# Performance work log

Hardware: AMD Instinct MI355X
Metric: run time of the kernel (lower is better)

Reference implementation:

```python
import jax, jax.numpy as jnp
import numpy as np

B, T1, T2, D = 16, 64, 64, 1024
PROJ = D // 2


def setup_inputs() -> dict:
    key = jax.random.key(0)
    k1, k2, k3 = jax.random.split(key, 3)
    x = jax.random.normal(k1, (B, T1, T2, D), dtype=jnp.float32)
    # glorot-style scale for params
    W_proj = jax.random.normal(k2, (D, PROJ), dtype=jnp.float32) * (2.0 / (D + PROJ)) ** 0.5
    v_score = jax.random.normal(k3, (PROJ,), dtype=jnp.float32) * (1.0 / PROJ) ** 0.5
    return {"x": x, "W_proj": W_proj, "v_score": v_score}


def reference(x, W_proj, v_score):
    # proj_input = tanh(tensordot(x, W_proj, axes=(3,0)))  -> (B, T1, T2, PROJ)
    proj = jnp.tanh(jnp.einsum('btsd,dp->btsp', x, W_proj))
    # att_scores = tensordot(proj, v_score, axes=(3,0))    -> (B, T1, T2)
    scores = jnp.einsum('btsp,p->bts', proj, v_score)
    # softmax over last axis (T2), weighted sum of x over T2 -> (B, T1, D)
    attn = jax.nn.softmax(scores, axis=-1)
    out = jnp.einsum('bts,btsd->btd', attn, x)
    return out
```

## Files before the change

kernel.cpp:

```cpp
#include <hip/hip_runtime.h>
#include <hip/hip_bf16.h>
#include <math.h>

#define B_    16
#define T1_   64
#define T2_   64
#define D_    1024
#define PROJ_ 512
#define BM    64
#define BK    32
#define NT    (D_ / BK)
#define LDP   40

typedef __attribute__((ext_vector_type(8))) short bf16x8;
typedef __attribute__((ext_vector_type(4))) float f32x4;
typedef __attribute__((ext_vector_type(4))) unsigned int u32x4;

__device__ __forceinline__ unsigned short f2bf(float f) {
  __hip_bfloat16 h = __float2bfloat16(f);
  return *reinterpret_cast<unsigned short*>(&h);
}

__global__ __launch_bounds__(256) void make_bfrag(
    const float* __restrict__ W, unsigned short* __restrict__ wt) {
  __shared__ float tile[32][33];
  const int t  = blockIdx.x;
  const int np = blockIdx.y;
  const int tx = threadIdx.x & 31;
  const int ty = threadIdx.x >> 5;
#pragma unroll
  for (int i = 0; i < 4; ++i)
    tile[ty + i * 8][tx] =
        W[(size_t)(t * 32 + ty + i * 8) * PROJ_ + np * 32 + tx];
  __syncthreads();
  if (threadIdx.x < 128) {
    const int sub  = threadIdx.x >> 6;
    const int lane = threadIdx.x & 63;
    const int llo = lane & 15, lhi = lane >> 4;
    unsigned short o[8];
#pragma unroll
    for (int j = 0; j < 8; ++j)
      o[j] = f2bf(tile[lhi * 8 + j][sub * 16 + llo]);
    const int n16 = np * 2 + sub;
    *(u32x4*)(wt + ((size_t)(t * 32 + n16) * 64 + lane) * 8) = *(const u32x4*)o;
  }
}

__global__ __launch_bounds__(512, 4) void fused_kernel(
    const float* __restrict__ x, const unsigned short* __restrict__ wt,
    const float* __restrict__ v, float* __restrict__ out) {
  __shared__ unsigned short As[2][BM][LDP];
  __shared__ float sp[BM][9];
  __shared__ float attn[BM];
  __shared__ f32x4 xred[256];

  const int tid  = threadIdx.x;
  const int lane = tid & 63;
  const int wid  = tid >> 6;
  const int llo  = lane & 15, lhi = lane >> 4;
  const int bt   = blockIdx.x;
  const int m0   = bt * BM;

  f32x4 acc[4][4];
#pragma unroll
  for (int mf = 0; mf < 4; ++mf)
#pragma unroll
    for (int nf = 0; nf < 4; ++nf) acc[mf][nf] = (f32x4){0.f, 0.f, 0.f, 0.f};

  const int arow = tid >> 3, akc = (tid & 7) * 4;
  const float* asrc = x + (size_t)(m0 + arow) * D_ + akc;

  const u32x4* wt4 = (const u32x4*)wt;
  const int bbase = (wid * 4) * 64 + lane;

  {
    float4 ra = *(const float4*)(asrc);
    ushort4 ua = {f2bf(ra.x), f2bf(ra.y), f2bf(ra.z), f2bf(ra.w)};
    *(ushort4*)&As[0][arow][akc] = ua;
  }
  u32x4 rb[4];
#pragma unroll
  for (int nf = 0; nf < 4; ++nf) rb[nf] = wt4[bbase + nf * 64];

#pragma unroll 2
  for (int t = 0; t < NT; ++t) {
    const int cur = t & 1;
    __syncthreads();

    float4 ra;
    if (t + 1 < NT) ra = *(const float4*)(asrc + (t + 1) * BK);

    bf16x8 af[4];
#pragma unroll
    for (int mf = 0; mf < 4; ++mf)
      af[mf] = *(const bf16x8*)&As[cur][mf * 16 + llo][lhi * 8];

#pragma unroll
    for (int nf = 0; nf < 4; ++nf) {
      bf16x8 bfr = *(const bf16x8*)&rb[nf];
#pragma unroll
      for (int mf = 0; mf < 4; ++mf)
        acc[mf][nf] = __builtin_amdgcn_mfma_f32_16x16x32_bf16(
            af[mf], bfr, acc[mf][nf], 0, 0, 0);
      if (t + 1 < NT)
        rb[nf] = wt4[bbase + (t + 1) * 2048 + nf * 64];
    }

    if (t + 1 < NT) {
      ushort4 ua = {f2bf(ra.x), f2bf(ra.y), f2bf(ra.z), f2bf(ra.w)};
      *(ushort4*)&As[cur ^ 1][arow][akc] = ua;
    }
  }

#pragma unroll
  for (int mf = 0; mf < 4; ++mf) {
    float pr[4] = {0.f, 0.f, 0.f, 0.f};
#pragma unroll
    for (int nf = 0; nf < 4; ++nf) {
      const float vv = v[wid * 64 + nf * 16 + llo];
#pragma unroll
      for (int r = 0; r < 4; ++r)
        pr[r] += tanhf(acc[mf][nf][r]) * vv;
    }
#pragma unroll
    for (int r = 0; r < 4; ++r) {
      float p = pr[r];
      p += __shfl_xor(p, 1, 64);
      p += __shfl_xor(p, 2, 64);
      p += __shfl_xor(p, 4, 64);
      p += __shfl_xor(p, 8, 64);
      if (llo == 0) sp[mf * 16 + lhi * 4 + r][wid] = p;
    }
  }
  __syncthreads();

  if (tid < BM) {
    float s = 0.f;
#pragma unroll
    for (int w = 0; w < 8; ++w) s += sp[tid][w];
    float mx = s;
#pragma unroll
    for (int mask = 1; mask < 64; mask <<= 1)
      mx = fmaxf(mx, __shfl_xor(mx, mask, 64));
    const float e = expf(s - mx);
    float sum = e;
#pragma unroll
    for (int mask = 1; mask < 64; mask <<= 1)
      sum += __shfl_xor(sum, mask, 64);
    attn[tid] = e / sum;
  }
  __syncthreads();

  const int c4 = tid & 255;
  const int sh = tid >> 8;
  const float* xg = x + (size_t)m0 * D_ + c4 * 4;
  f32x4 o = {0.f, 0.f, 0.f, 0.f};
#pragma unroll 4
  for (int s = sh * 32; s < sh * 32 + 32; ++s) {
    const float w = attn[s];
    const float4 xv = *(const float4*)(xg + (size_t)s * D_);
    o[0] += w * xv.x; o[1] += w * xv.y; o[2] += w * xv.z; o[3] += w * xv.w;
  }
  if (sh == 1) xred[c4] = o;
  __syncthreads();
  if (sh == 0) {
    f32x4 o2 = xred[c4];
    float4 res = {o[0] + o2[0], o[1] + o2[1], o[2] + o2[2], o[3] + o2[3]};
    *(float4*)(out + (size_t)bt * D_ + c4 * 4) = res;
  }
}

extern "C" void kernel_launch(void* const* d_in, const int* in_sizes, int n_in,
                              void* d_out, int out_size, void* d_ws, size_t ws_size,
                              hipStream_t stream) {
  const float* x = (const float*)d_in[0];
  const float* W = (const float*)d_in[1];
  const float* v = (const float*)d_in[2];
  float* out = (float*)d_out;
  unsigned short* Wt = (unsigned short*)d_ws;

  make_bfrag<<<dim3(NT, PROJ_ / 32), 256, 0, stream>>>(W, Wt);
  fused_kernel<<<B_ * T1_, 512, 0, stream>>>(x, Wt, v, out);
}
```

Before: 127.7 us.

## Deepen A prefetch, use fast tanh/exp intrinsics, split weighted-sum accumulators

Prefetches the x tile two K-steps ahead using alternating register buffers in a manually unrolled loop. Replaces library tanhf, expf and division with exp2/rcp hardware intrinsics, and swaps the bf16 conversion for a bit-trick round-to-nearest-even. The final weighted sum now uses four independent accumulators with all loads issued up front to expose more memory-level parallelism. This trades some accuracy in tanh (and loses NaN handling in the conversion) for fewer instructions, and the extra prefetch registers may raise register pressure.

```diff
diff --git a/kernel.cpp b/kernel.cpp
--- a/kernel.cpp
+++ b/kernel.cpp
@@ -17,8 +17,14 @@
 typedef __attribute__((ext_vector_type(4))) unsigned int u32x4;
 
 __device__ __forceinline__ unsigned short f2bf(float f) {
-  __hip_bfloat16 h = __float2bfloat16(f);
-  return *reinterpret_cast<unsigned short*>(&h);
+  unsigned int u = __builtin_bit_cast(unsigned int, f);
+  u += 0x7FFFu + ((u >> 16) & 1u);
+  return (unsigned short)(u >> 16);
+}
+
+__device__ __forceinline__ float fast_tanh(float a) {
+  float t = __builtin_amdgcn_exp2f(a * 2.885390081777927f);
+  return 1.0f - 2.0f * __builtin_amdgcn_rcpf(t + 1.0f);
 }
 
 __global__ __launch_bounds__(256) void make_bfrag(
@@ -73,54 +79,58 @@
   const u32x4* wt4 = (const u32x4*)wt;
   const int bbase = (wid * 4) * 64 + lane;
 
+  float4 s0 = *(const float4*)(asrc);
+  float4 s1 = *(const float4*)(asrc + BK);
+  u32x4 rb[4];
+#pragma unroll
+  for (int nf = 0; nf < 4; ++nf) rb[nf] = wt4[bbase + nf * 64];
   {
-    float4 ra = *(const float4*)(asrc);
-    ushort4 ua = {f2bf(ra.x), f2bf(ra.y), f2bf(ra.z), f2bf(ra.w)};
+    ushort4 ua = {f2bf(s0.x), f2bf(s0.y), f2bf(s0.z), f2bf(s0.w)};
     *(ushort4*)&As[0][arow][akc] = ua;
   }
-  u32x4 rb[4];
-#pragma unroll
-  for (int nf = 0; nf < 4; ++nf) rb[nf] = wt4[bbase + nf * 64];
-
-#pragma unroll 2
-  for (int t = 0; t < NT; ++t) {
-    const int cur = t & 1;
-    __syncthreads();
-
-    float4 ra;
-    if (t + 1 < NT) ra = *(const float4*)(asrc + (t + 1) * BK);
-
-    bf16x8 af[4];
-#pragma unroll
-    for (int mf = 0; mf < 4; ++mf)
-      af[mf] = *(const bf16x8*)&As[cur][mf * 16 + llo][lhi * 8];
-
-#pragma unroll
-    for (int nf = 0; nf < 4; ++nf) {
-      bf16x8 bfr = *(const bf16x8*)&rb[nf];
-#pragma unroll
-      for (int mf = 0; mf < 4; ++mf)
-        acc[mf][nf] = __builtin_amdgcn_mfma_f32_16x16x32_bf16(
-            af[mf], bfr, acc[mf][nf], 0, 0, 0);
-      if (t + 1 < NT)
-        rb[nf] = wt4[bbase + (t + 1) * 2048 + nf * 64];
-    }
-
-    if (t + 1 < NT) {
-      ushort4 ua = {f2bf(ra.x), f2bf(ra.y), f2bf(ra.z), f2bf(ra.w)};
-      *(ushort4*)&As[cur ^ 1][arow][akc] = ua;
-    }
-  }
-
+
+#define KSTEP(T, SLD, SCV, BR, BW)                                           \
+  {                                                                          \
+    __syncthreads();                                                         \
+    bf16x8 af0 = *(const bf16x8*)&As[BR][ 0 + llo][lhi * 8];                 \
+    bf16x8 af1 = *(const bf16x8*)&As[BR][16 + llo][lhi * 8];                 \
+    bf16x8 af2 = *(const bf16x8*)&As[BR][32 + llo][lhi * 8];                 \
+    bf16x8 af3 = *(const bf16x8*)&As[BR][48 + llo][lhi * 8];                 \
+    if ((T) + 2 < NT) SLD = *(const float4*)(asrc + ((T) + 2) * BK);         \
+    _Pragma("unroll")                                                        \
+    for (int nf = 0; nf < 4; ++nf) {                                         \
+      bf16x8 bfr = *(const bf16x8*)&rb[nf];                                  \
+      acc[0][nf] = __builtin_amdgcn_mfma_f32_16x16x32_bf16(af0, bfr, acc[0][nf], 0, 0, 0); \
+      acc[1][nf] = __builtin_amdgcn_mfma_f32_16x16x32_bf16(af1, bfr, acc[1][nf], 0, 0, 0); \
+      acc[2][nf] = __builtin_amdgcn_mfma_f32_16x16x32_bf16(af2, bfr, acc[2][nf], 0, 0, 0); \
+      acc[3][nf] = __builtin_amdgcn_mfma_f32_16x16x32_bf16(af3, bfr, acc[3][nf], 0, 0, 0); \
+      if ((T) + 1 < NT) rb[nf] = wt4[bbase + ((T) + 1) * 2048 + nf * 64];    \
+    }                                                                        \
+    if ((T) + 1 < NT) {                                                      \
+      ushort4 ua = {f2bf(SCV.x), f2bf(SCV.y), f2bf(SCV.z), f2bf(SCV.w)};     \
+      *(ushort4*)&As[BW][arow][akc] = ua;                                    \
+    }                                                                        \
+  }
+
+  for (int t = 0; t < NT; t += 2) {
+    KSTEP(t,     s0, s1, 0, 1)
+    KSTEP(t + 1, s1, s0, 1, 0)
+  }
+#undef KSTEP
+
+  float vv0 = v[wid * 64 +  0 + llo];
+  float vv1 = v[wid * 64 + 16 + llo];
+  float vv2 = v[wid * 64 + 32 + llo];
+  float vv3 = v[wid * 64 + 48 + llo];
 #pragma unroll
   for (int mf = 0; mf < 4; ++mf) {
     float pr[4] = {0.f, 0.f, 0.f, 0.f};
 #pragma unroll
-    for (int nf = 0; nf < 4; ++nf) {
-      const float vv = v[wid * 64 + nf * 16 + llo];
-#pragma unroll
-      for (int r = 0; r < 4; ++r)
-        pr[r] += tanhf(acc[mf][nf][r]) * vv;
+    for (int r = 0; r < 4; ++r) {
+      pr[r] += fast_tanh(acc[mf][0][r]) * vv0;
+      pr[r] += fast_tanh(acc[mf][1][r]) * vv1;
+      pr[r] += fast_tanh(acc[mf][2][r]) * vv2;
+      pr[r] += fast_tanh(acc[mf][3][r]) * vv3;
     }
 #pragma unroll
     for (int r = 0; r < 4; ++r) {
@@ -142,30 +152,42 @@
 #pragma unroll
     for (int mask = 1; mask < 64; mask <<= 1)
       mx = fmaxf(mx, __shfl_xor(mx, mask, 64));
-    const float e = expf(s - mx);
+    const float e = __builtin_amdgcn_exp2f((s - mx) * 1.442695040888963f);
     float sum = e;
 #pragma unroll
     for (int mask = 1; mask < 64; mask <<= 1)
       sum += __shfl_xor(sum, mask, 64);
-    attn[tid] = e / sum;
+    attn[tid] = e * __builtin_amdgcn_rcpf(sum);
   }
   __syncthreads();
 
   const int c4 = tid & 255;
   const int sh = tid >> 8;
-  const float* xg = x + (size_t)m0 * D_ + c4 * 4;
-  f32x4 o = {0.f, 0.f, 0.f, 0.f};
-#pragma unroll 4
-  for (int s = sh * 32; s < sh * 32 + 32; ++s) {
-    const float w = attn[s];
-    const float4 xv = *(const float4*)(xg + (size_t)s * D_);
-    o[0] += w * xv.x; o[1] += w * xv.y; o[2] += w * xv.z; o[3] += w * xv.w;
-  }
+  const float* xg = x + ((size_t)m0 + sh * 32) * D_ + c4 * 4;
+  f32x4 o0 = {0.f,0.f,0.f,0.f}, o1 = o0, o2 = o0, o3 = o0;
+#pragma unroll
+  for (int s = 0; s < 32; s += 4) {
+    const float w0 = attn[sh * 32 + s + 0];
+    const float w1 = attn[sh * 32 + s + 1];
+    const float w2 = attn[sh * 32 + s + 2];
+    const float w3 = attn[sh * 32 + s + 3];
+    const float4 a0 = *(const float4*)(xg + (size_t)(s + 0) * D_);
+    const float4 a1 = *(const float4*)(xg + (size_t)(s + 1) * D_);
+    const float4 a2 = *(const float4*)(xg + (size_t)(s + 2) * D_);
+    const float4 a3 = *(const float4*)(xg + (size_t)(s + 3) * D_);
+    o0[0] += w0 * a0.x; o0[1] += w0 * a0.y; o0[2] += w0 * a0.z; o0[3] += w0 * a0.w;
+    o1[0] += w1 * a1.x; o1[1] += w1 * a1.y; o1[2] += w1 * a1.z; o1[3] += w1 * a1.w;
+    o2[0] += w2 * a2.x; o2[1] += w2 * a2.y; o2[2] += w2 * a2.z; o2[3] += w2 * a2.w;
+    o3[0] += w3 * a3.x; o3[1] += w3 * a3.y; o3[2] += w3 * a3.z; o3[3] += w3 * a3.w;
+  }
+  f32x4 o;
+#pragma unroll
+  for (int j = 0; j < 4; ++j) o[j] = (o0[j] + o1[j]) + (o2[j] + o3[j]);
   if (sh == 1) xred[c4] = o;
   __syncthreads();
   if (sh == 0) {
-    f32x4 o2 = xred[c4];
-    float4 res = {o[0] + o2[0], o[1] + o2[1], o[2] + o2[2], o[3] + o2[3]};
+    f32x4 o2b = xred[c4];
+    float4 res = {o[0] + o2b[0], o[1] + o2b[1], o[2] + o2b[2], o[3] + o2b[3]};
     *(float4*)(out + (size_t)bt * D_ + c4 * 4) = res;
   }
 }
```

Result: faster. 113.9 us (-10.8%).
